# Performance work log

Measured on AMD Instinct MI355X. Metric: run time of the kernel, lower is better.

The kernel has to match this reference:

```python
import jax, jax.numpy as jnp
import numpy as np

B, C, D = 512, 100000, 512
MARGIN = 0.5  # ArcFace-style additive angular margin


def setup_inputs() -> dict:
    key = jax.random.key(0)
    k1, k2, k3 = jax.random.split(key, 3)
    embeddings = jax.random.normal(k1, (B, D), dtype=jnp.float32)
    labels = jax.random.randint(k2, (B,), 0, C, dtype=jnp.int32)
    weight = 0.01 * jax.random.normal(k3, (C, D), dtype=jnp.float32)  # torch.normal(0, 0.01, (C, D))
    return {"embeddings": embeddings, "labels": labels, "weight": weight}


def _l2_normalize(x, eps=1e-12):
    return x / jnp.maximum(jnp.linalg.norm(x, axis=-1, keepdims=True), eps)


def reference(embeddings, labels, weight):
    cos_m = jnp.cos(MARGIN)
    sin_m = jnp.sin(MARGIN)

    e = _l2_normalize(embeddings)          # (B, D)
    w = _l2_normalize(weight)              # (C, D)
    logits = jnp.clip(jnp.einsum('bd,cd->bc', e, w), -1.0, 1.0)  # (B, C) cosines

    bsz, ncls = logits.shape
    rows = jnp.arange(bsz)
    cos_t = logits[rows, labels]                                   # (B,) cos(theta_y)
    sin_t = jnp.sqrt(jnp.clip(1.0 - cos_t * cos_t, 0.0, None))     # sin(theta_y)
    cos_tm = cos_t * cos_m - sin_t * sin_m                         # cos(theta_y + m)
    sin_tm = sin_t * cos_m + cos_t * sin_m                         # sin(theta_y + m)

    # non-target class indices per row, ascending, skipping the target: (B, C-1)
    base = jnp.arange(ncls - 1)[None, :]
    nt_idx = base + (base >= labels[:, None]).astype(base.dtype)

    # margin_softmax: logits2 = cos(theta_j) - cos(theta_y + m) over non-target j
    nt_logits = jnp.take_along_axis(logits, nt_idx, axis=1)       # (B, C-1)
    logits2 = nt_logits - cos_tm[:, None]

    # no_grad block: weight_m is unit-norm point at angle theta_y+m from e,
    # so ||w_j - w_m||^2 = 2 - 2 <w_j, w_m>  (avoids materializing (B, C, D)).
    w_y = w[labels]                                                # (B, D)
    w_m = (-sin_m * e + sin_tm[:, None] * w_y) / sin_t[:, None]    # (B, D), unit norm
    sim = jnp.einsum('bd,cd->bc', w_m, w)                          # (B, C)
    nt_sim = jnp.take_along_axis(sim, nt_idx, axis=1)              # (B, C-1)
    diff_weight_norm = jax.lax.stop_gradient(
        jnp.sqrt(jnp.clip(2.0 - 2.0 * nt_sim, 0.0, None)))         # (B, C-1)

    e_logits = jnp.sum(jnp.exp(logits2 / diff_weight_norm), axis=1)  # (B,)
    return jnp.mean(jnp.log1p(e_logits))
```

## Files before the change

### kernel.cpp

```cpp
#include <hip/hip_runtime.h>
#include <hip/hip_fp8.h>
#include <math.h>

#define B_SZ 512
#define C_SZ 100000
#define D_SZ 512

#define BM 128
#define BN 128
#define BK 64
#define NTILES 782
#define MT 8
#define NBLK (NTILES * MT)
#define KSTEPS 8
#define DEPTH 2

typedef __attribute__((ext_vector_type(4))) float f32x4;
typedef __attribute__((ext_vector_type(16))) float f32x16;
typedef __attribute__((ext_vector_type(4))) int i32x4;
typedef __attribute__((ext_vector_type(8))) int i32x8;

#define UNITY_SCALE 0x7F7F7F7F

__device__ __forceinline__ void gload_lds16(const void* gptr, void* lptr) {
  __builtin_amdgcn_global_load_lds(
      (const __attribute__((address_space(1))) void*)gptr,
      (__attribute__((address_space(3))) void*)lptr,
      16, 0, 0);
}

__device__ __forceinline__ unsigned char f2fp8(float x) {
  __hip_fp8_e4m3 h(x);
  return (unsigned char)h.__x;
}
__device__ __forceinline__ float fp82f(unsigned int u) {
  __hip_fp8_e4m3 h;
  h.__x = (unsigned char)u;
  return (float)h;
}
__device__ __forceinline__ unsigned int pack4f8(float a, float b, float c, float d) {
  return (unsigned int)f2fp8(a) | ((unsigned int)f2fp8(b) << 8) |
         ((unsigned int)f2fp8(c) << 16) | ((unsigned int)f2fp8(d) << 24);
}

__device__ __forceinline__ i32x8 ld_frag(const unsigned char* base, int frag, int l) {
  i32x4 lo = *(const i32x4*)(base + frag * 2048 + l * 16);
  i32x4 hg = *(const i32x4*)(base + frag * 2048 + 1024 + l * 16);
  return __builtin_shufflevector(lo, hg, 0, 1, 2, 3, 4, 5, 6, 7);
}

__global__ __launch_bounds__(256) void k_norm_w(const float* __restrict__ w,
                                                unsigned char* __restrict__ w8) {
  const int row = blockIdx.x * 4 + (threadIdx.x >> 6);
  const int lane = threadIdx.x & 63;
  const float4* wr = (const float4*)(w + (size_t)row * D_SZ);
  float4 v0 = wr[lane];
  float4 v1 = wr[64 + lane];
  float ss = v0.x*v0.x + v0.y*v0.y + v0.z*v0.z + v0.w*v0.w
           + v1.x*v1.x + v1.y*v1.y + v1.z*v1.z + v1.w*v1.w;
  #pragma unroll
  for (int o = 32; o; o >>= 1) ss += __shfl_xor(ss, o, 64);
  const float rn = __builtin_amdgcn_rsqf(fmaxf(ss, 1e-24f));
  unsigned int* out = (unsigned int*)(w8 + (size_t)row * D_SZ);
  out[lane] = pack4f8(v0.x * rn, v0.y * rn, v0.z * rn, v0.w * rn);
  out[64 + lane] = pack4f8(v1.x * rn, v1.y * rn, v1.z * rn, v1.w * rn);
}

__global__ __launch_bounds__(64) void k_prep(const float* __restrict__ e,
                                             const int* __restrict__ labels,
                                             const unsigned char* __restrict__ w8,
                                             unsigned char* __restrict__ A8f,
                                             float4* __restrict__ params) {
  const int b = blockIdx.x;
  const int lane = threadIdx.x;
  const float4* er = (const float4*)(e + (size_t)b * D_SZ);
  float4 v0 = er[lane], v1 = er[64 + lane];
  float ss = v0.x*v0.x + v0.y*v0.y + v0.z*v0.z + v0.w*v0.w
           + v1.x*v1.x + v1.y*v1.y + v1.z*v1.z + v1.w*v1.w;
  #pragma unroll
  for (int o = 32; o; o >>= 1) ss += __shfl_xor(ss, o, 64);
  const float rn = __builtin_amdgcn_rsqf(fmaxf(ss, 1e-24f));
  v0.x *= rn; v0.y *= rn; v0.z *= rn; v0.w *= rn;
  v1.x *= rn; v1.y *= rn; v1.z *= rn; v1.w *= rn;

  const unsigned int ue0 = pack4f8(v0.x, v0.y, v0.z, v0.w);
  const unsigned int ue1 = pack4f8(v1.x, v1.y, v1.z, v1.w);

  const int lab = labels[b];
  const unsigned int* wr = (const unsigned int*)(w8 + (size_t)lab * D_SZ);
  const unsigned int w0 = wr[lane], w1 = wr[64 + lane];

  const int re = 2 * b;
  const int frag = re >> 5;
  const int rife = re & 31;
  const int wk = (4 * lane) & 63;
  const int ks = lane >> 4;
  const int sbits = (((wk >> 5) & 1) << 5) | (((wk >> 4) & 1) << 6);
  const int byteo = wk & 15;
  unsigned char* fb = A8f + (size_t)frag * 16384;
  unsigned char* pe = fb + (rife | sbits) * 16 + byteo;
  unsigned char* pw = fb + ((rife + 1) | sbits) * 16 + byteo;
  *(unsigned int*)(pe + ks * 2048) = ue0;
  *(unsigned int*)(pe + (ks + 4) * 2048) = ue1;
  *(unsigned int*)(pw + ks * 2048) = w0;
  *(unsigned int*)(pw + (ks + 4) * 2048) = w1;

  float d = v0.x * fp82f(w0 & 255) + v0.y * fp82f((w0 >> 8) & 255)
          + v0.z * fp82f((w0 >> 16) & 255) + v0.w * fp82f(w0 >> 24)
          + v1.x * fp82f(w1 & 255) + v1.y * fp82f((w1 >> 8) & 255)
          + v1.z * fp82f((w1 >> 16) & 255) + v1.w * fp82f(w1 >> 24);
  #pragma unroll
  for (int o = 32; o; o >>= 1) d += __shfl_xor(d, o, 64);

  if (lane == 0) {
    const float cos_m = 0.877582561890372716f;
    const float sin_m = 0.479425538604203000f;
    float cos_t = fminf(fmaxf(d, -1.0f), 1.0f);
    float sin_t = sqrtf(fmaxf(1.0f - cos_t * cos_t, 0.0f));
    float cos_tm = cos_t * cos_m - sin_t * sin_m;
    float sin_tm = sin_t * cos_m + cos_t * sin_m;
    float inv_st = 1.0f / fmaxf(sin_t, 1e-20f);
    params[b] = make_float4(cos_tm, sin_m * inv_st, sin_tm * inv_st, 0.0f);
  }
}

__device__ __forceinline__ float termf(float de, float dwy, float4 p, bool kill) {
  float c = fminf(fmaxf(de, -1.0f), 1.0f);
  float s = p.z * dwy - p.y * de;
  float x = fmaxf(fmaf(-2.0f, s, 2.0f), 1e-20f);
  float t = (c - p.x) * __builtin_amdgcn_rsqf(x);
  float r = __expf(t);
  return kill ? 0.0f : r;
}

__global__ __launch_bounds__(512, 6) void k_gemm(const unsigned char* __restrict__ A8f,
                                                 const unsigned char* __restrict__ W8,
                                                 const float4* __restrict__ params,
                                                 const int* __restrict__ labels,
                                                 float* __restrict__ part) {
  __shared__ __align__(32) unsigned char Bt[DEPTH][BN * BK];
  __shared__ float ered[64];
  __shared__ float4 pl[64];
  __shared__ int ll[64];

  const int bid = blockIdx.x;
  const int p = (bid & 7) * (NBLK / 8) + (bid >> 3);
  const int nt = p >> 3, mt = p & 7;
  const int t = threadIdx.x;
  const int w = t >> 6, l = t & 63;
  const int n0 = nt * BN;
  const int b0 = mt * 64;

  if (t < 64) {
    ered[t] = 0.0f;
    pl[t] = params[b0 + t];
    ll[t] = labels[b0 + t];
  }

  const int kpart = ((t >> 5) & 1) * 32 + ((t >> 6) & 1) * 16;
  int brow_s = n0 + (t >> 7) * 32 + (t & 31);
  if (brow_s >= C_SZ) brow_s = C_SZ - 1;
  const int boffs = brow_s * D_SZ + kpart;

  const unsigned char* afb =
      A8f + (size_t)(mt * 4 + (w & 3)) * 16384 + l * 16;

  f32x16 accA = {}, accB = {};
  const int fA = w & 3;
  const int fB0 = (w >> 2) * 2;
  const int hi = l >> 5;

#define STAGE(d, ts)                                                        \
  gload_lds16(W8 + (size_t)(boffs + (ts) * BK), (void*)(Bt[d] + t * 16))

  STAGE(0, 0);
  STAGE(1, 1);
  asm volatile("s_waitcnt vmcnt(1) lgkmcnt(0)" ::: "memory");
  __builtin_amdgcn_s_barrier();

  #pragma unroll
  for (int s = 0; s < KSTEPS; ++s) {
    const int d = s & 1;
    i32x4 alo = *(const i32x4*)(afb + s * 2048);
    i32x4 ahi = *(const i32x4*)(afb + s * 2048 + 1024);
    i32x8 av = __builtin_shufflevector(alo, ahi, 0, 1, 2, 3, 4, 5, 6, 7);
    i32x8 bv = ld_frag(Bt[d], fB0, l);
    __builtin_amdgcn_s_setprio(1);
    accA = __builtin_amdgcn_mfma_scale_f32_32x32x64_f8f6f4(
        av, bv, accA, 0, 0, 0, UNITY_SCALE, 0, UNITY_SCALE);
    bv = ld_frag(Bt[d], fB0 + 1, l);
    accB = __builtin_amdgcn_mfma_scale_f32_32x32x64_f8f6f4(
        av, bv, accB, 0, 0, 0, UNITY_SCALE, 0, UNITY_SCALE);
    __builtin_amdgcn_s_setprio(0);
    if (s < KSTEPS - 1) {
      asm volatile("s_waitcnt vmcnt(0)" ::: "memory");
      __builtin_amdgcn_s_barrier();
      if (s + 2 < KSTEPS)
        STAGE(d, s + 2);
    }
  }
#undef STAGE

  #pragma unroll
  for (int rp = 0; rp < 8; ++rp) {
    const int r = 2 * rp;
    const int lb = fA * 16 + (rp & 1) + 4 * (rp >> 1) + 2 * hi;
    float4 pp = pl[lb];
    int lab = ll[lb];
    int j0 = n0 + fB0 * 32 + (l & 31);
    int j1 = j0 + 32;
    float s = termf(accA[r], accA[r + 1], pp, (j0 >= C_SZ) || (j0 == lab))
            + termf(accB[r], accB[r + 1], pp, (j1 >= C_SZ) || (j1 == lab));
    #pragma unroll
    for (int o = 1; o < 32; o <<= 1) s += __shfl_xor(s, o, 64);
    if ((l & 31) == 0) atomicAdd(&ered[lb], s);
  }
  __syncthreads();
  if (t < 64) part[(size_t)(b0 + t) * NTILES + nt] = ered[t];
}

__global__ __launch_bounds__(256) void k_rowsum(const float* __restrict__ part,
                                                float* __restrict__ rowsum) {
  const int b = blockIdx.x;
  float s = 0.0f;
  for (int i = threadIdx.x; i < NTILES; i += 256) s += part[(size_t)b * NTILES + i];
  #pragma unroll
  for (int o = 32; o; o >>= 1) s += __shfl_xor(s, o, 64);
  __shared__ float red[4];
  if ((threadIdx.x & 63) == 0) red[threadIdx.x >> 6] = s;
  __syncthreads();
  if (threadIdx.x == 0)
    rowsum[b] = log1pf(red[0] + red[1] + red[2] + red[3]);
}

__global__ __launch_bounds__(512) void k_final(const float* __restrict__ rowsum,
                                               float* __restrict__ out) {
  const int b = threadIdx.x;
  float v = rowsum[b];
  __shared__ float red[512];
  red[b] = v;
  __syncthreads();
  #pragma unroll
  for (int o = 256; o; o >>= 1) {
    if (b < o) red[b] += red[b + o];
    __syncthreads();
  }
  if (b == 0) out[0] = red[0] / (float)B_SZ;
}

extern "C" void kernel_launch(void* const* d_in, const int* in_sizes, int n_in,
                              void* d_out, int out_size, void* d_ws, size_t ws_size,
                              hipStream_t stream) {
  const float* emb = (const float*)d_in[0];
  const int* labels = (const int*)d_in[1];
  const float* w = (const float*)d_in[2];

  char* ws = (char*)d_ws;
  unsigned char* w8 = (unsigned char*)ws;
  size_t off = (size_t)C_SZ * D_SZ;
  unsigned char* A8f = (unsigned char*)(ws + off);
  off += (size_t)2 * B_SZ * D_SZ;
  float4* params = (float4*)(ws + off);
  off += (size_t)B_SZ * 16;
  float* part = (float*)(ws + off);
  off += (size_t)B_SZ * NTILES * 4;
  float* rowsum = (float*)(ws + off);
  off += (size_t)B_SZ * 4;

  k_norm_w<<<dim3(C_SZ / 4), dim3(256), 0, stream>>>(w, w8);
  k_prep<<<dim3(B_SZ), dim3(64), 0, stream>>>(emb, labels, w8, A8f, params);
  k_gemm<<<dim3(NBLK), dim3(512), 0, stream>>>(A8f, w8, params, labels, part);
  k_rowsum<<<dim3(B_SZ), dim3(256), 0, stream>>>(part, rowsum);
  k_final<<<dim3(1), dim3(512), 0, stream>>>(rowsum, (float*)d_out);
}
```

Measured before the change: 135.4 us.

## Stage B tile in two half-K chunks instead of double-buffered per-K pipeline

Replaces the depth-2 per-K-step B staging with two big stages, each loading half of K (four k-steps) into a 32 KB LDS buffer. This cuts the per-step waitcnt and barrier synchronisation from seven rounds to two, and issues more loads at once. In exchange it grows LDS per block from 16 KB to 32 KB, which may lower occupancy, and gives up overlap of loads with MFMA inside each half.

```diff
diff --git a/kernel.cpp b/kernel.cpp
--- a/kernel.cpp
+++ b/kernel.cpp
@@ -6,14 +6,11 @@
 #define C_SZ 100000
 #define D_SZ 512
 
-#define BM 128
 #define BN 128
-#define BK 64
 #define NTILES 782
 #define MT 8
 #define NBLK (NTILES * MT)
 #define KSTEPS 8
-#define DEPTH 2
 
 typedef __attribute__((ext_vector_type(4))) float f32x4;
 typedef __attribute__((ext_vector_type(16))) float f32x16;
@@ -46,6 +43,11 @@
 __device__ __forceinline__ i32x8 ld_frag(const unsigned char* base, int frag, int l) {
   i32x4 lo = *(const i32x4*)(base + frag * 2048 + l * 16);
   i32x4 hg = *(const i32x4*)(base + frag * 2048 + 1024 + l * 16);
+  return __builtin_shufflevector(lo, hg, 0, 1, 2, 3, 4, 5, 6, 7);
+}
+__device__ __forceinline__ i32x8 ld_a(const unsigned char* p) {
+  i32x4 lo = *(const i32x4*)(p);
+  i32x4 hg = *(const i32x4*)(p + 1024);
   return __builtin_shufflevector(lo, hg, 0, 1, 2, 3, 4, 5, 6, 7);
 }
 
@@ -138,7 +140,7 @@
                                                  const float4* __restrict__ params,
                                                  const int* __restrict__ labels,
                                                  float* __restrict__ part) {
-  __shared__ __align__(32) unsigned char Bt[DEPTH][BN * BK];
+  __shared__ __align__(32) unsigned char Bt[4 * 4 * 2048];
   __shared__ float ered[64];
   __shared__ float4 pl[64];
   __shared__ int ll[64];
@@ -157,10 +159,21 @@
     ll[t] = labels[b0 + t];
   }
 
-  const int kpart = ((t >> 5) & 1) * 32 + ((t >> 6) & 1) * 16;
-  int brow_s = n0 + (t >> 7) * 32 + (t & 31);
-  if (brow_s >= C_SZ) brow_s = C_SZ - 1;
-  const int boffs = brow_s * D_SZ + kpart;
+#define STAGE_HALF(h)                                                       \
+  do {                                                                      \
+    _Pragma("unroll")                                                       \
+    for (int i = 0; i < 4; ++i) {                                           \
+      const int g = i * 512 + t;                                            \
+      const int kst = g >> 9;                                               \
+      const int fr = (g >> 7) & 3;                                          \
+      const int s_ = g & 127;                                               \
+      int row = n0 + fr * 32 + (s_ & 31);                                   \
+      if (row >= C_SZ) row = C_SZ - 1;                                      \
+      const int kk = (h) * 256 + kst * 64 +                                 \
+                     ((s_ >> 5) & 1) * 32 + ((s_ >> 6) & 1) * 16;           \
+      gload_lds16(W8 + (size_t)row * D_SZ + kk, (void*)(Bt + g * 16));      \
+    }                                                                       \
+  } while (0)
 
   const unsigned char* afb =
       A8f + (size_t)(mt * 4 + (w & 3)) * 16384 + l * 16;
@@ -170,36 +183,45 @@
   const int fB0 = (w >> 2) * 2;
   const int hi = l >> 5;
 
-#define STAGE(d, ts)                                                        \
-  gload_lds16(W8 + (size_t)(boffs + (ts) * BK), (void*)(Bt[d] + t * 16))
-
-  STAGE(0, 0);
-  STAGE(1, 1);
-  asm volatile("s_waitcnt vmcnt(1) lgkmcnt(0)" ::: "memory");
+  STAGE_HALF(0);
+  asm volatile("s_waitcnt vmcnt(0) lgkmcnt(0)" ::: "memory");
   __builtin_amdgcn_s_barrier();
 
   #pragma unroll
-  for (int s = 0; s < KSTEPS; ++s) {
-    const int d = s & 1;
-    i32x4 alo = *(const i32x4*)(afb + s * 2048);
-    i32x4 ahi = *(const i32x4*)(afb + s * 2048 + 1024);
-    i32x8 av = __builtin_shufflevector(alo, ahi, 0, 1, 2, 3, 4, 5, 6, 7);
-    i32x8 bv = ld_frag(Bt[d], fB0, l);
+  for (int sl = 0; sl < 4; ++sl) {
+    const int s = sl;
+    i32x8 av = ld_a(afb + s * 2048);
+    const unsigned char* bb = Bt + sl * 8192;
+    i32x8 bv = ld_frag(bb, fB0, l);
     __builtin_amdgcn_s_setprio(1);
     accA = __builtin_amdgcn_mfma_scale_f32_32x32x64_f8f6f4(
         av, bv, accA, 0, 0, 0, UNITY_SCALE, 0, UNITY_SCALE);
-    bv = ld_frag(Bt[d], fB0 + 1, l);
+    bv = ld_frag(bb, fB0 + 1, l);
     accB = __builtin_amdgcn_mfma_scale_f32_32x32x64_f8f6f4(
         av, bv, accB, 0, 0, 0, UNITY_SCALE, 0, UNITY_SCALE);
     __builtin_amdgcn_s_setprio(0);
-    if (s < KSTEPS - 1) {
-      asm volatile("s_waitcnt vmcnt(0)" ::: "memory");
-      __builtin_amdgcn_s_barrier();
-      if (s + 2 < KSTEPS)
-        STAGE(d, s + 2);
-    }
-  }
-#undef STAGE
+  }
+
+  __builtin_amdgcn_s_barrier();
+  STAGE_HALF(1);
+  asm volatile("s_waitcnt vmcnt(0) lgkmcnt(0)" ::: "memory");
+  __builtin_amdgcn_s_barrier();
+
+  #pragma unroll
+  for (int sl = 0; sl < 4; ++sl) {
+    const int s = 4 + sl;
+    i32x8 av = ld_a(afb + s * 2048);
+    const unsigned char* bb = Bt + sl * 8192;
+    i32x8 bv = ld_frag(bb, fB0, l);
+    __builtin_amdgcn_s_setprio(1);
+    accA = __builtin_amdgcn_mfma_scale_f32_32x32x64_f8f6f4(
+        av, bv, accA, 0, 0, 0, UNITY_SCALE, 0, UNITY_SCALE);
+    bv = ld_frag(bb, fB0 + 1, l);
+    accB = __builtin_amdgcn_mfma_scale_f32_32x32x64_f8f6f4(
+        av, bv, accB, 0, 0, 0, UNITY_SCALE, 0, UNITY_SCALE);
+    __builtin_amdgcn_s_setprio(0);
+  }
+#undef STAGE_HALF
 
   #pragma unroll
   for (int rp = 0; rp < 8; ++rp) {
```

Result: slower. 292.1 us (+115.7%).
